# Kernel optimization log

Measured on AMD Instinct MI355X. Metric: run time of the kernel, lower is better.

## Reference

```python
import jax, jax.numpy as jnp
import numpy as np


def axisangle2mat(p):
    # p: [N, 6] = (rotation vector rx,ry,rz, translation tx,ty,tz) -> [N, 3, 4]
    v = p[:, :3]
    t = p[:, 3:]
    theta = jnp.sqrt(jnp.sum(v * v, axis=-1) + 1e-12)  # [N]
    k = v / theta[:, None]
    kx, ky, kz = k[:, 0], k[:, 1], k[:, 2]
    zero = jnp.zeros_like(kx)
    K = jnp.stack([
        jnp.stack([zero, -kz, ky], -1),
        jnp.stack([kz, zero, -kx], -1),
        jnp.stack([-ky, kx, zero], -1),
    ], -2)  # [N,3,3]
    I = jnp.eye(3, dtype=p.dtype)
    s = jnp.sin(theta)[:, None, None]
    c = (1.0 - jnp.cos(theta))[:, None, None]
    R = I + s * K + c * jnp.matmul(K, K)
    return jnp.concatenate([R, t[:, :, None]], axis=-1)  # [N,3,4]


def grid_sample_3d(vol, grid):
    # vol: [D,H,W]; grid: [...,3] with last dim (x,y,z) in [-1,1].
    # Replicates F.grid_sample(mode='bilinear', padding_mode='zeros', align_corners=False).
    D, H, W = vol.shape
    ix = ((grid[..., 0] + 1.0) * W - 1.0) * 0.5
    iy = ((grid[..., 1] + 1.0) * H - 1.0) * 0.5
    iz = ((grid[..., 2] + 1.0) * D - 1.0) * 0.5
    x0 = jnp.floor(ix); y0 = jnp.floor(iy); z0 = jnp.floor(iz)
    fx = ix - x0; fy = iy - y0; fz = iz - z0
    vol_flat = vol.reshape(-1)
    out = jnp.zeros(grid.shape[:-1], vol.dtype)
    for dz in (0, 1):
        for dy in (0, 1):
            for dx in (0, 1):
                xc = x0 + dx; yc = y0 + dy; zc = z0 + dz
                wgt = ((fx if dx else 1.0 - fx) * (fy if dy else 1.0 - fy) * (fz if dz else 1.0 - fz))
                valid = ((xc >= 0) & (xc < W) & (yc >= 0) & (yc < H) & (zc >= 0) & (zc < D))
                xi = jnp.clip(xc, 0, W - 1).astype(jnp.int32)
                yi = jnp.clip(yc, 0, H - 1).astype(jnp.int32)
                zi = jnp.clip(zc, 0, D - 1).astype(jnp.int32)
                v = vol_flat[(zi * H + yi) * W + xi]
                out = out + jnp.where(valid, v * wgt, 0.0)
    return out


def setup_inputs() -> dict:
    key = jax.random.key(0)
    ks = jax.random.split(key, 8)
    B, n, D, H, W = 4096, 2048, 256, 256, 256
    x = jax.random.normal(ks[0], (1, 1, D, H, W), dtype=jnp.float32)
    # voxel-space sample points inside the volume
    sampleGrid = jax.random.uniform(ks[1], (B, 3), dtype=jnp.float32) * jnp.array([W - 1, H - 1, D - 1], jnp.float32)
    ax = jnp.concatenate([
        jax.random.normal(ks[2], (B, 1, 3), dtype=jnp.float32) * 0.1,   # small rotations
        jax.random.normal(ks[3], (B, 1, 3), dtype=jnp.float32) * 5.0,   # translations (voxels)
    ], axis=-1)
    low = jax.random.uniform(ks[4], (B, 1, 3), dtype=jnp.float32) * 2.0
    ext = jax.random.uniform(ks[5], (B, 1, 3), dtype=jnp.float32) * 4.0 + 1.0
    bound = jnp.concatenate([low, low + ext], axis=1)  # [B,2,3], bound[:,1] > bound[:,0]
    A = jax.random.normal(ks[6], (B, 3, 3), dtype=jnp.float32) * 0.3
    InvCovScaled = jnp.einsum('bij,bkj->bik', A, A) + 0.5 * jnp.eye(3, dtype=jnp.float32)  # SPD
    xyz_psf = jax.random.normal(ks[7], (B, n, 3), dtype=jnp.float32)
    psf_sigma = jnp.ones((1,), jnp.float32)  # unused in forward (as in the original)
    return dict(x=x, sampleGrid=sampleGrid, ax=ax, bound=bound,
                InvCovScaled=InvCovScaled, psf_sigma=psf_sigma, xyz_psf=xyz_psf)


def reference(x, sampleGrid, ax, bound, InvCovScaled, psf_sigma, xyz_psf):
    # x: [1,1,D,H,W]; sampleGrid: [B,3]; ax: [B,1,6]; bound: [B,2,3];
    # InvCovScaled: [B,3,3]; xyz_psf: [B,n,3] (the torch.randn draw, made explicit)
    W = x.shape[-1]; H = x.shape[-2]; D = x.shape[-3]
    size = (W, H, D)  # matches torch: size = [x.shape[-1], x.shape[-2], x.shape[-3]]
    scaled_xyz_psf = 2.0 * jax.nn.sigmoid(xyz_psf) - 1.0                      # [B,n,3]
    half = (bound[:, 1, :] - bound[:, 0, :]) * 0.5                            # [B,3]
    bound_psf = scaled_xyz_psf * half[:, None]                                # [B,n,3]
    mat = axisangle2mat(ax.reshape(-1, 6)).reshape(ax.shape[:-1] + (3, 4))    # [B,1,3,4]
    R = mat[:, 0, :, :3]                                                      # [B,3,3]
    T = mat[:, 0, :, 3]                                                       # [B,3]
    # trans_first=True: R @ (p + T)
    mat_sampleGrid = jnp.einsum('bij,bj->bi', R, sampleGrid + T)[:, None]     # [B,1,3]
    psf_sampleGrid = mat_sampleGrid + bound_psf                               # [B,n,3]
    norm = jnp.array([size[0] - 1, size[1] - 1, size[2] - 1], psf_sampleGrid.dtype)
    grid = 2.0 * (psf_sampleGrid / norm - 0.5)
    psf_x = grid_sample_3d(x[0, 0], grid)                                     # [B,n]
    # Mahalanobis-style weights: exp(-0.5 * c^T InvCov c)
    q = jnp.einsum('bni,bij,bnj->bn', bound_psf, InvCovScaled, bound_psf)
    w = jnp.exp(-0.5 * q)                                                     # [B,n]
    y = jnp.sum(psf_x * w, axis=-1) / jnp.sum(w, axis=-1)                     # [B]
    return y
```

## Files before the change

kernel.cpp:

```cpp
#include <hip/hip_runtime.h>
#include <math.h>

constexpr int NT   = 256;
constexpr int DIMV = 256;
constexpr int RS   = 8;
constexpr int RROW = 9;
constexpr int RSLICE = RS * RROW;

__device__ __forceinline__ float rflf(float x) {
    return __uint_as_float(__builtin_amdgcn_readfirstlane(__float_as_uint(x)));
}
__device__ __forceinline__ float fexp2(float x) {
#if __has_builtin(__builtin_amdgcn_exp2f)
    return __builtin_amdgcn_exp2f(x);
#else
    return __expf(x * 0.6931471805599453f);
#endif
}

__global__ __launch_bounds__(NT, 6) void psf_sample_kernel(
    const float* __restrict__ vol,
    const float* __restrict__ sampleGrid,
    const float* __restrict__ ax,
    const float* __restrict__ bound,
    const float* __restrict__ invcov,
    const float* __restrict__ xyz,
    float* __restrict__ out,
    int n)
{
    const int b   = blockIdx.x;
    const int tid = threadIdx.x;

    __shared__ float s_vol[RS * RSLICE];
    __shared__ float s_red[2 * (NT / 64)];

    const float v0 = ax[b*6+0], v1 = ax[b*6+1], v2 = ax[b*6+2];
    const float t0 = ax[b*6+3], t1 = ax[b*6+4], t2 = ax[b*6+5];
    const float theta = sqrtf(v0*v0 + v1*v1 + v2*v2 + 1e-12f);
    const float inv = 1.0f / theta;
    const float kx = v0*inv, ky = v1*inv, kz = v2*inv;
    const float sn = sinf(theta);
    const float cn = 1.0f - cosf(theta);
    const float R00 = 1.0f - cn*(ky*ky + kz*kz);
    const float R01 = -sn*kz + cn*kx*ky;
    const float R02 =  sn*ky + cn*kx*kz;
    const float R10 =  sn*kz + cn*kx*ky;
    const float R11 = 1.0f - cn*(kx*kx + kz*kz);
    const float R12 = -sn*kx + cn*ky*kz;
    const float R20 = -sn*ky + cn*kx*kz;
    const float R21 =  sn*kx + cn*ky*kz;
    const float R22 = 1.0f - cn*(kx*kx + ky*ky);
    const float g0 = sampleGrid[b*3+0] + t0;
    const float g1 = sampleGrid[b*3+1] + t1;
    const float g2 = sampleGrid[b*3+2] + t2;
    const float ms0 = R00*g0 + R01*g1 + R02*g2;
    const float ms1 = R10*g0 + R11*g1 + R12*g2;
    const float ms2 = R20*g0 + R21*g1 + R22*g2;
    const float h0 = (bound[b*6+3] - bound[b*6+0]) * 0.5f;
    const float h1 = (bound[b*6+4] - bound[b*6+1]) * 0.5f;
    const float h2 = (bound[b*6+5] - bound[b*6+2]) * 0.5f;
    const float M00 = invcov[b*9+0], M01 = invcov[b*9+1], M02 = invcov[b*9+2];
    const float M11 = invcov[b*9+4], M12 = invcov[b*9+5], M22 = invcov[b*9+8];

    const float LOG2E = 1.4426950408889634f;
    const float Bxx = rflf(-0.5f * M00 * h0 * h0 * LOG2E);
    const float Byy = rflf(-0.5f * M11 * h1 * h1 * LOG2E);
    const float Bzz = rflf(-0.5f * M22 * h2 * h2 * LOG2E);
    const float Bxy = rflf(-M01 * h0 * h1 * LOG2E);
    const float Bxz = rflf(-M02 * h0 * h2 * LOG2E);
    const float Byz = rflf(-M12 * h1 * h2 * LOG2E);

    const float kk = 256.0f / 255.0f;
    const float cix = rflf(fmaf(ms0, kk, -0.5f));
    const float ciy = rflf(fmaf(ms1, kk, -0.5f));
    const float ciz = rflf(fmaf(ms2, kk, -0.5f));
    const float hx = rflf(h0 * kk);
    const float hy = rflf(h1 * kk);
    const float hz = rflf(h2 * kk);

    const int bx = __builtin_amdgcn_readfirstlane((int)floorf(cix - hx - 1e-3f));
    const int by = __builtin_amdgcn_readfirstlane((int)floorf(ciy - hy - 1e-3f));
    const int bz = __builtin_amdgcn_readfirstlane((int)floorf(ciz - hz - 1e-3f));
    const float addrC = rflf((float)(bz * RSLICE + by * RROW + bx));
    const bool fast = (hx <= 2.9f) && (hy <= 2.9f) && (hz <= 2.9f);

    if (fast) {
        #pragma unroll
        for (int pass = 0; pass < (RS*RS*RS)/NT; ++pass) {
            const int idx = pass * NT + tid;
            const int lx = idx & 7, ly = (idx >> 3) & 7, lz = idx >> 6;
            const int gx = bx + lx, gy = by + ly, gz = bz + lz;
            float v = 0.0f;
            if ((unsigned)gx < (unsigned)DIMV && (unsigned)gy < (unsigned)DIMV &&
                (unsigned)gz < (unsigned)DIMV)
                v = vol[((size_t)gz * DIMV + gy) * DIMV + gx];
            s_vol[(lz * RS + ly) * RROW + lx] = v;
        }
    }
    __syncthreads();

    float sum_wx = 0.0f, sum_w = 0.0f;

    auto doSample = [&](float rx, float ry, float rz) {
        const float ex = fexp2(rx * -LOG2E);
        const float ey = fexp2(ry * -LOG2E);
        const float ez = fexp2(rz * -LOG2E);
        const float sx = (1.0f - ex) * __builtin_amdgcn_rcpf(1.0f + ex);
        const float sy = (1.0f - ey) * __builtin_amdgcn_rcpf(1.0f + ey);
        const float sz = (1.0f - ez) * __builtin_amdgcn_rcpf(1.0f + ez);

        const float ixf = fmaf(sx, hx, cix);
        const float iyf = fmaf(sy, hy, ciy);
        const float izf = fmaf(sz, hz, ciz);
        const float x0f = floorf(ixf), y0f = floorf(iyf), z0f = floorf(izf);
        const float fx = ixf - x0f, fy = iyf - y0f, fz = izf - z0f;

        float val;
        if (fast) {
            const float ef = fmaf(z0f, (float)RSLICE,
                             fmaf(y0f, (float)RROW, x0f - addrC));
            const int e = (int)ef;
            const float* p = &s_vol[e];
            const float v000 = p[0],              v001 = p[1];
            const float v010 = p[RROW],           v011 = p[RROW + 1];
            const float v100 = p[RSLICE],         v101 = p[RSLICE + 1];
            const float v110 = p[RSLICE + RROW],  v111 = p[RSLICE + RROW + 1];
            const float a00 = fmaf(fx, v001 - v000, v000);
            const float a01 = fmaf(fx, v011 - v010, v010);
            const float a10 = fmaf(fx, v101 - v100, v100);
            const float a11 = fmaf(fx, v111 - v110, v110);
            const float a0  = fmaf(fy, a01 - a00, a00);
            const float a1  = fmaf(fy, a11 - a10, a10);
            val = fmaf(fz, a1 - a0, a0);
        } else {
            const int x0 = (int)x0f, y0 = (int)y0f, z0 = (int)z0f;
            const int x1 = x0 + 1, y1 = y0 + 1, z1 = z0 + 1;
            const bool vx0 = (unsigned)x0 < (unsigned)DIMV;
            const bool vx1 = (unsigned)x1 < (unsigned)DIMV;
            const bool vy0 = (unsigned)y0 < (unsigned)DIMV;
            const bool vy1 = (unsigned)y1 < (unsigned)DIMV;
            const bool vz0 = (unsigned)z0 < (unsigned)DIMV;
            const bool vz1 = (unsigned)z1 < (unsigned)DIMV;
            const int cx0 = min(max(x0,0),DIMV-1), cx1 = min(max(x1,0),DIMV-1);
            const int cy0 = min(max(y0,0),DIMV-1), cy1 = min(max(y1,0),DIMV-1);
            const int cz0 = min(max(z0,0),DIMV-1), cz1 = min(max(z1,0),DIMV-1);
            const float wx0 = 1.0f-fx, wx1 = fx, wy0 = 1.0f-fy, wy1 = fy;
            const float wz0 = 1.0f-fz, wz1 = fz;
            const int r00 = (cz0*DIMV + cy0)*DIMV, r01 = (cz0*DIMV + cy1)*DIMV;
            const int r10 = (cz1*DIMV + cy0)*DIMV, r11 = (cz1*DIMV + cy1)*DIMV;
            val  = (vz0&&vy0&&vx0) ? vol[r00+cx0]*(wz0*wy0*wx0) : 0.0f;
            val += (vz0&&vy0&&vx1) ? vol[r00+cx1]*(wz0*wy0*wx1) : 0.0f;
            val += (vz0&&vy1&&vx0) ? vol[r01+cx0]*(wz0*wy1*wx0) : 0.0f;
            val += (vz0&&vy1&&vx1) ? vol[r01+cx1]*(wz0*wy1*wx1) : 0.0f;
            val += (vz1&&vy0&&vx0) ? vol[r10+cx0]*(wz1*wy0*wx0) : 0.0f;
            val += (vz1&&vy0&&vx1) ? vol[r10+cx1]*(wz1*wy0*wx1) : 0.0f;
            val += (vz1&&vy1&&vx0) ? vol[r11+cx0]*(wz1*wy1*wx0) : 0.0f;
            val += (vz1&&vy1&&vx1) ? vol[r11+cx1]*(wz1*wy1*wx1) : 0.0f;
        }

        const float f = fmaf(Bxx, sx*sx,
                        fmaf(Byy, sy*sy,
                        fmaf(Bzz, sz*sz,
                        fmaf(Bxy, sx*sy,
                        fmaf(Bxz, sx*sz, Byz * (sy*sz))))));
        const float w = fexp2(f);
        sum_w  += w;
        sum_wx = fmaf(w, val, sum_wx);
    };

    const int ng = n >> 2;
    const float4* __restrict__ xb4 =
        reinterpret_cast<const float4*>(xyz + (size_t)b * n * 3);
    for (int g = tid; g < ng; g += 2*NT) {
        const float4 a0 = xb4[g*3 + 0];
        const float4 a1 = xb4[g*3 + 1];
        const float4 a2 = xb4[g*3 + 2];
        const int g2 = g + NT;
        const bool has2 = g2 < ng;
        float4 c0, c1, c2;
        if (has2) { c0 = xb4[g2*3 + 0]; c1 = xb4[g2*3 + 1]; c2 = xb4[g2*3 + 2]; }
        doSample(a0.x, a0.y, a0.z);
        doSample(a0.w, a1.x, a1.y);
        doSample(a1.z, a1.w, a2.x);
        doSample(a2.y, a2.z, a2.w);
        if (has2) {
            doSample(c0.x, c0.y, c0.z);
            doSample(c0.w, c1.x, c1.y);
            doSample(c1.z, c1.w, c2.x);
            doSample(c2.y, c2.z, c2.w);
        }
    }
    const float* __restrict__ xb = xyz + (size_t)b * n * 3;
    for (int i = (ng << 2) + tid; i < n; i += NT)
        doSample(xb[i*3+0], xb[i*3+1], xb[i*3+2]);

    #pragma unroll
    for (int off = 32; off > 0; off >>= 1) {
        sum_wx += __shfl_down(sum_wx, off);
        sum_w  += __shfl_down(sum_w,  off);
    }
    const int wave = tid >> 6;
    const int lane = tid & 63;
    if (lane == 0) { s_red[wave*2] = sum_wx; s_red[wave*2+1] = sum_w; }
    __syncthreads();
    if (tid == 0) {
        float twx = 0.0f, tw = 0.0f;
        #pragma unroll
        for (int wv = 0; wv < NT/64; ++wv) { twx += s_red[wv*2]; tw += s_red[wv*2+1]; }
        out[b] = twx / tw;
    }
}

extern "C" void kernel_launch(void* const* d_in, const int* in_sizes, int n_in,
                              void* d_out, int out_size, void* d_ws, size_t ws_size,
                              hipStream_t stream) {
    const float* vol        = (const float*)d_in[0];
    const float* sampleGrid = (const float*)d_in[1];
    const float* ax         = (const float*)d_in[2];
    const float* bound      = (const float*)d_in[3];
    const float* invcov     = (const float*)d_in[4];
    const float* xyz        = (const float*)d_in[6];
    float* out              = (float*)d_out;

    const int B = in_sizes[1] / 3;
    const int n = in_sizes[6] / (B * 3);

    psf_sample_kernel<<<B, NT, 0, stream>>>(vol, sampleGrid, ax, bound, invcov,
                                            xyz, out, n);
}
```

Baseline: 30.74 us.

## Assign one wavefront per batch element instead of one block per element

Each 256-thread block now handles four batch elements, one per wavefront. Each wave loads its own 8x8x8 shared-memory volume patch and reduces with shuffles only, so the cross-wave shared-memory reduction and second barrier go away. The grid shrinks by four and each wave processes all 2048 samples of its element serially across 64 lanes. Launch bounds drop the occupancy hint from 6 to 4 blocks. The gain is less per-block setup and synchronisation, at the cost of longer per-wave work and possibly different latency hiding.

```diff
diff --git a/kernel.cpp b/kernel.cpp
--- a/kernel.cpp
+++ b/kernel.cpp
@@ -2,6 +2,7 @@
 #include <math.h>
 
 constexpr int NT   = 256;
+constexpr int WPB  = 4;
 constexpr int DIMV = 256;
 constexpr int RS   = 8;
 constexpr int RROW = 9;
@@ -18,7 +19,7 @@
 #endif
 }
 
-__global__ __launch_bounds__(NT, 6) void psf_sample_kernel(
+__global__ __launch_bounds__(NT, 4) void psf_sample_kernel(
     const float* __restrict__ vol,
     const float* __restrict__ sampleGrid,
     const float* __restrict__ ax,
@@ -26,188 +27,182 @@
     const float* __restrict__ invcov,
     const float* __restrict__ xyz,
     float* __restrict__ out,
-    int n)
+    int n, int B)
 {
-    const int b   = blockIdx.x;
-    const int tid = threadIdx.x;
-
-    __shared__ float s_vol[RS * RSLICE];
-    __shared__ float s_red[2 * (NT / 64)];
-
-    const float v0 = ax[b*6+0], v1 = ax[b*6+1], v2 = ax[b*6+2];
-    const float t0 = ax[b*6+3], t1 = ax[b*6+4], t2 = ax[b*6+5];
-    const float theta = sqrtf(v0*v0 + v1*v1 + v2*v2 + 1e-12f);
-    const float inv = 1.0f / theta;
-    const float kx = v0*inv, ky = v1*inv, kz = v2*inv;
-    const float sn = sinf(theta);
-    const float cn = 1.0f - cosf(theta);
-    const float R00 = 1.0f - cn*(ky*ky + kz*kz);
-    const float R01 = -sn*kz + cn*kx*ky;
-    const float R02 =  sn*ky + cn*kx*kz;
-    const float R10 =  sn*kz + cn*kx*ky;
-    const float R11 = 1.0f - cn*(kx*kx + kz*kz);
-    const float R12 = -sn*kx + cn*ky*kz;
-    const float R20 = -sn*ky + cn*kx*kz;
-    const float R21 =  sn*kx + cn*ky*kz;
-    const float R22 = 1.0f - cn*(kx*kx + ky*ky);
-    const float g0 = sampleGrid[b*3+0] + t0;
-    const float g1 = sampleGrid[b*3+1] + t1;
-    const float g2 = sampleGrid[b*3+2] + t2;
-    const float ms0 = R00*g0 + R01*g1 + R02*g2;
-    const float ms1 = R10*g0 + R11*g1 + R12*g2;
-    const float ms2 = R20*g0 + R21*g1 + R22*g2;
-    const float h0 = (bound[b*6+3] - bound[b*6+0]) * 0.5f;
-    const float h1 = (bound[b*6+4] - bound[b*6+1]) * 0.5f;
-    const float h2 = (bound[b*6+5] - bound[b*6+2]) * 0.5f;
-    const float M00 = invcov[b*9+0], M01 = invcov[b*9+1], M02 = invcov[b*9+2];
-    const float M11 = invcov[b*9+4], M12 = invcov[b*9+5], M22 = invcov[b*9+8];
+    const int tid  = threadIdx.x;
+    const int wid  = tid >> 6;
+    const int lane = tid & 63;
+    const int b    = blockIdx.x * WPB + wid;
+    const bool valid = b < B;
+
+    __shared__ float s_vol[WPB][RS * RSLICE];
 
     const float LOG2E = 1.4426950408889634f;
-    const float Bxx = rflf(-0.5f * M00 * h0 * h0 * LOG2E);
-    const float Byy = rflf(-0.5f * M11 * h1 * h1 * LOG2E);
-    const float Bzz = rflf(-0.5f * M22 * h2 * h2 * LOG2E);
-    const float Bxy = rflf(-M01 * h0 * h1 * LOG2E);
-    const float Bxz = rflf(-M02 * h0 * h2 * LOG2E);
-    const float Byz = rflf(-M12 * h1 * h2 * LOG2E);
-
-    const float kk = 256.0f / 255.0f;
-    const float cix = rflf(fmaf(ms0, kk, -0.5f));
-    const float ciy = rflf(fmaf(ms1, kk, -0.5f));
-    const float ciz = rflf(fmaf(ms2, kk, -0.5f));
-    const float hx = rflf(h0 * kk);
-    const float hy = rflf(h1 * kk);
-    const float hz = rflf(h2 * kk);
-
-    const int bx = __builtin_amdgcn_readfirstlane((int)floorf(cix - hx - 1e-3f));
-    const int by = __builtin_amdgcn_readfirstlane((int)floorf(ciy - hy - 1e-3f));
-    const int bz = __builtin_amdgcn_readfirstlane((int)floorf(ciz - hz - 1e-3f));
-    const float addrC = rflf((float)(bz * RSLICE + by * RROW + bx));
-    const bool fast = (hx <= 2.9f) && (hy <= 2.9f) && (hz <= 2.9f);
-
-    if (fast) {
-        #pragma unroll
-        for (int pass = 0; pass < (RS*RS*RS)/NT; ++pass) {
-            const int idx = pass * NT + tid;
-            const int lx = idx & 7, ly = (idx >> 3) & 7, lz = idx >> 6;
-            const int gx = bx + lx, gy = by + ly, gz = bz + lz;
-            float v = 0.0f;
-            if ((unsigned)gx < (unsigned)DIMV && (unsigned)gy < (unsigned)DIMV &&
-                (unsigned)gz < (unsigned)DIMV)
-                v = vol[((size_t)gz * DIMV + gy) * DIMV + gx];
-            s_vol[(lz * RS + ly) * RROW + lx] = v;
+    float cix, ciy, ciz, hx, hy, hz, addrC;
+    float Bxx, Byy, Bzz, Bxy, Bxz, Byz;
+    int bx = 0, by = 0, bz = 0;
+    bool fast = false;
+    float h0 = 0, h1 = 0, h2 = 0;
+
+    if (valid) {
+        const float v0 = ax[b*6+0], v1 = ax[b*6+1], v2 = ax[b*6+2];
+        const float t0 = ax[b*6+3], t1 = ax[b*6+4], t2 = ax[b*6+5];
+        const float theta = sqrtf(v0*v0 + v1*v1 + v2*v2 + 1e-12f);
+        const float inv = 1.0f / theta;
+        const float kx = v0*inv, ky = v1*inv, kz = v2*inv;
+        const float sn = sinf(theta);
+        const float cn = 1.0f - cosf(theta);
+        const float R00 = 1.0f - cn*(ky*ky + kz*kz);
+        const float R01 = -sn*kz + cn*kx*ky;
+        const float R02 =  sn*ky + cn*kx*kz;
+        const float R10 =  sn*kz + cn*kx*ky;
+        const float R11 = 1.0f - cn*(kx*kx + kz*kz);
+        const float R12 = -sn*kx + cn*ky*kz;
+        const float R20 = -sn*ky + cn*kx*kz;
+        const float R21 =  sn*kx + cn*ky*kz;
+        const float R22 = 1.0f - cn*(kx*kx + ky*ky);
+        const float g0 = sampleGrid[b*3+0] + t0;
+        const float g1 = sampleGrid[b*3+1] + t1;
+        const float g2 = sampleGrid[b*3+2] + t2;
+        const float ms0 = R00*g0 + R01*g1 + R02*g2;
+        const float ms1 = R10*g0 + R11*g1 + R12*g2;
+        const float ms2 = R20*g0 + R21*g1 + R22*g2;
+        h0 = (bound[b*6+3] - bound[b*6+0]) * 0.5f;
+        h1 = (bound[b*6+4] - bound[b*6+1]) * 0.5f;
+        h2 = (bound[b*6+5] - bound[b*6+2]) * 0.5f;
+        const float M00 = invcov[b*9+0], M01 = invcov[b*9+1], M02 = invcov[b*9+2];
+        const float M11 = invcov[b*9+4], M12 = invcov[b*9+5], M22 = invcov[b*9+8];
+
+        Bxx = rflf(-0.5f * M00 * h0 * h0 * LOG2E);
+        Byy = rflf(-0.5f * M11 * h1 * h1 * LOG2E);
+        Bzz = rflf(-0.5f * M22 * h2 * h2 * LOG2E);
+        Bxy = rflf(-M01 * h0 * h1 * LOG2E);
+        Bxz = rflf(-M02 * h0 * h2 * LOG2E);
+        Byz = rflf(-M12 * h1 * h2 * LOG2E);
+
+        const float kk = 256.0f / 255.0f;
+        cix = rflf(fmaf(ms0, kk, -0.5f));
+        ciy = rflf(fmaf(ms1, kk, -0.5f));
+        ciz = rflf(fmaf(ms2, kk, -0.5f));
+        hx  = rflf(h0 * kk);
+        hy  = rflf(h1 * kk);
+        hz  = rflf(h2 * kk);
+
+        bx = __builtin_amdgcn_readfirstlane((int)floorf(cix - hx - 1e-3f));
+        by = __builtin_amdgcn_readfirstlane((int)floorf(ciy - hy - 1e-3f));
+        bz = __builtin_amdgcn_readfirstlane((int)floorf(ciz - hz - 1e-3f));
+        addrC = rflf((float)(bz * RSLICE + by * RROW + bx));
+        fast = (hx <= 2.9f) && (hy <= 2.9f) && (hz <= 2.9f);
+
+        if (fast) {
+            #pragma unroll
+            for (int pass = 0; pass < (RS*RS*RS)/64; ++pass) {
+                const int idx = pass * 64 + lane;
+                const int lx = idx & 7, ly = (idx >> 3) & 7, lz = idx >> 6;
+                const int gx = bx + lx, gy = by + ly, gz = bz + lz;
+                float v = 0.0f;
+                if ((unsigned)gx < (unsigned)DIMV && (unsigned)gy < (unsigned)DIMV &&
+                    (unsigned)gz < (unsigned)DIMV)
+                    v = vol[((size_t)gz * DIMV + gy) * DIMV + gx];
+                s_vol[wid][(lz * RS + ly) * RROW + lx] = v;
+            }
         }
     }
     __syncthreads();
 
-    float sum_wx = 0.0f, sum_w = 0.0f;
-
-    auto doSample = [&](float rx, float ry, float rz) {
-        const float ex = fexp2(rx * -LOG2E);
-        const float ey = fexp2(ry * -LOG2E);
-        const float ez = fexp2(rz * -LOG2E);
-        const float sx = (1.0f - ex) * __builtin_amdgcn_rcpf(1.0f + ex);
-        const float sy = (1.0f - ey) * __builtin_amdgcn_rcpf(1.0f + ey);
-        const float sz = (1.0f - ez) * __builtin_amdgcn_rcpf(1.0f + ez);
-
-        const float ixf = fmaf(sx, hx, cix);
-        const float iyf = fmaf(sy, hy, ciy);
-        const float izf = fmaf(sz, hz, ciz);
-        const float x0f = floorf(ixf), y0f = floorf(iyf), z0f = floorf(izf);
-        const float fx = ixf - x0f, fy = iyf - y0f, fz = izf - z0f;
-
-        float val;
-        if (fast) {
-            const float ef = fmaf(z0f, (float)RSLICE,
-                             fmaf(y0f, (float)RROW, x0f - addrC));
-            const int e = (int)ef;
-            const float* p = &s_vol[e];
-            const float v000 = p[0],              v001 = p[1];
-            const float v010 = p[RROW],           v011 = p[RROW + 1];
-            const float v100 = p[RSLICE],         v101 = p[RSLICE + 1];
-            const float v110 = p[RSLICE + RROW],  v111 = p[RSLICE + RROW + 1];
-            const float a00 = fmaf(fx, v001 - v000, v000);
-            const float a01 = fmaf(fx, v011 - v010, v010);
-            const float a10 = fmaf(fx, v101 - v100, v100);
-            const float a11 = fmaf(fx, v111 - v110, v110);
-            const float a0  = fmaf(fy, a01 - a00, a00);
-            const float a1  = fmaf(fy, a11 - a10, a10);
-            val = fmaf(fz, a1 - a0, a0);
-        } else {
-            const int x0 = (int)x0f, y0 = (int)y0f, z0 = (int)z0f;
-            const int x1 = x0 + 1, y1 = y0 + 1, z1 = z0 + 1;
-            const bool vx0 = (unsigned)x0 < (unsigned)DIMV;
-            const bool vx1 = (unsigned)x1 < (unsigned)DIMV;
-            const bool vy0 = (unsigned)y0 < (unsigned)DIMV;
-            const bool vy1 = (unsigned)y1 < (unsigned)DIMV;
-            const bool vz0 = (unsigned)z0 < (unsigned)DIMV;
-            const bool vz1 = (unsigned)z1 < (unsigned)DIMV;
-            const int cx0 = min(max(x0,0),DIMV-1), cx1 = min(max(x1,0),DIMV-1);
-            const int cy0 = min(max(y0,0),DIMV-1), cy1 = min(max(y1,0),DIMV-1);
-            const int cz0 = min(max(z0,0),DIMV-1), cz1 = min(max(z1,0),DIMV-1);
-            const float wx0 = 1.0f-fx, wx1 = fx, wy0 = 1.0f-fy, wy1 = fy;
-            const float wz0 = 1.0f-fz, wz1 = fz;
-            const int r00 = (cz0*DIMV + cy0)*DIMV, r01 = (cz0*DIMV + cy1)*DIMV;
-            const int r10 = (cz1*DIMV + cy0)*DIMV, r11 = (cz1*DIMV + cy1)*DIMV;
-            val  = (vz0&&vy0&&vx0) ? vol[r00+cx0]*(wz0*wy0*wx0) : 0.0f;
-            val += (vz0&&vy0&&vx1) ? vol[r00+cx1]*(wz0*wy0*wx1) : 0.0f;
-            val += (vz0&&vy1&&vx0) ? vol[r01+cx0]*(wz0*wy1*wx0) : 0.0f;
-            val += (vz0&&vy1&&vx1) ? vol[r01+cx1]*(wz0*wy1*wx1) : 0.0f;
-            val += (vz1&&vy0&&vx0) ? vol[r10+cx0]*(wz1*wy0*wx0) : 0.0f;
-            val += (vz1&&vy0&&vx1) ? vol[r10+cx1]*(wz1*wy0*wx1) : 0.0f;
-            val += (vz1&&vy1&&vx0) ? vol[r11+cx0]*(wz1*wy1*wx0) : 0.0f;
-            val += (vz1&&vy1&&vx1) ? vol[r11+cx1]*(wz1*wy1*wx1) : 0.0f;
+    if (valid) {
+        float sum_wx = 0.0f, sum_w = 0.0f;
+        const float* __restrict__ sreg = s_vol[wid];
+
+        auto doSample = [&](float rx, float ry, float rz) {
+            const float ex = fexp2(rx * -LOG2E);
+            const float ey = fexp2(ry * -LOG2E);
+            const float ez = fexp2(rz * -LOG2E);
+            const float sx = (1.0f - ex) * __builtin_amdgcn_rcpf(1.0f + ex);
+            const float sy = (1.0f - ey) * __builtin_amdgcn_rcpf(1.0f + ey);
+            const float sz = (1.0f - ez) * __builtin_amdgcn_rcpf(1.0f + ez);
+
+            const float ixf = fmaf(sx, hx, cix);
+            const float iyf = fmaf(sy, hy, ciy);
+            const float izf = fmaf(sz, hz, ciz);
+            const float x0f = floorf(ixf), y0f = floorf(iyf), z0f = floorf(izf);
+            const float fx = ixf - x0f, fy = iyf - y0f, fz = izf - z0f;
+
+            float val;
+            if (fast) {
+                const float ef = fmaf(z0f, (float)RSLICE,
+                                 fmaf(y0f, (float)RROW, x0f - addrC));
+                const int e = (int)ef;
+                const float* p = &sreg[e];
+                const float v000 = p[0],              v001 = p[1];
+                const float v010 = p[RROW],           v011 = p[RROW + 1];
+                const float v100 = p[RSLICE],         v101 = p[RSLICE + 1];
+                const float v110 = p[RSLICE + RROW],  v111 = p[RSLICE + RROW + 1];
+                const float a00 = fmaf(fx, v001 - v000, v000);
+                const float a01 = fmaf(fx, v011 - v010, v010);
+                const float a10 = fmaf(fx, v101 - v100, v100);
+                const float a11 = fmaf(fx, v111 - v110, v110);
+                const float a0  = fmaf(fy, a01 - a00, a00);
+                const float a1  = fmaf(fy, a11 - a10, a10);
+                val = fmaf(fz, a1 - a0, a0);
+            } else {
+                const int x0 = (int)x0f, y0 = (int)y0f, z0 = (int)z0f;
+                const int x1 = x0 + 1, y1 = y0 + 1, z1 = z0 + 1;
+                const bool vx0 = (unsigned)x0 < (unsigned)DIMV;
+                const bool vx1 = (unsigned)x1 < (unsigned)DIMV;
+                const bool vy0 = (unsigned)y0 < (unsigned)DIMV;
+                const bool vy1 = (unsigned)y1 < (unsigned)DIMV;
+                const bool vz0 = (unsigned)z0 < (unsigned)DIMV;
+                const bool vz1 = (unsigned)z1 < (unsigned)DIMV;
+                const int cx0 = min(max(x0,0),DIMV-1), cx1 = min(max(x1,0),DIMV-1);
+                const int cy0 = min(max(y0,0),DIMV-1), cy1 = min(max(y1,0),DIMV-1);
+                const int cz0 = min(max(z0,0),DIMV-1), cz1 = min(max(z1,0),DIMV-1);
+                const float wx0 = 1.0f-fx, wx1 = fx, wy0 = 1.0f-fy, wy1 = fy;
+                const float wz0 = 1.0f-fz, wz1 = fz;
+                const int r00 = (cz0*DIMV + cy0)*DIMV, r01 = (cz0*DIMV + cy1)*DIMV;
+                const int r10 = (cz1*DIMV + cy0)*DIMV, r11 = (cz1*DIMV + cy1)*DIMV;
+                val  = (vz0&&vy0&&vx0) ? vol[r00+cx0]*(wz0*wy0*wx0) : 0.0f;
+                val += (vz0&&vy0&&vx1) ? vol[r00+cx1]*(wz0*wy0*wx1) : 0.0f;
+                val += (vz0&&vy1&&vx0) ? vol[r01+cx0]*(wz0*wy1*wx0) : 0.0f;
+                val += (vz0&&vy1&&vx1) ? vol[r01+cx1]*(wz0*wy1*wx1) : 0.0f;
+                val += (vz1&&vy0&&vx0) ? vol[r10+cx0]*(wz1*wy0*wx0) : 0.0f;
+                val += (vz1&&vy0&&vx1) ? vol[r10+cx1]*(wz1*wy0*wx1) : 0.0f;
+                val += (vz1&&vy1&&vx0) ? vol[r11+cx0]*(wz1*wy1*wx0) : 0.0f;
+                val += (vz1&&vy1&&vx1) ? vol[r11+cx1]*(wz1*wy1*wx1) : 0.0f;
+            }
+
+            const float f = fmaf(Bxx, sx*sx,
+                            fmaf(Byy, sy*sy,
+                            fmaf(Bzz, sz*sz,
+                            fmaf(Bxy, sx*sy,
+                            fmaf(Bxz, sx*sz, Byz * (sy*sz))))));
+            const float w = fexp2(f);
+            sum_w  += w;
+            sum_wx = fmaf(w, val, sum_wx);
+        };
+
+        const int ng = n >> 2;
+        const float4* __restrict__ xb4 =
+            reinterpret_cast<const float4*>(xyz + (size_t)b * n * 3);
+        for (int g = lane; g < ng; g += 64) {
+            const float4 q0 = xb4[g*3 + 0];
+            const float4 q1 = xb4[g*3 + 1];
+            const float4 q2 = xb4[g*3 + 2];
+            doSample(q0.x, q0.y, q0.z);
+            doSample(q0.w, q1.x, q1.y);
+            doSample(q1.z, q1.w, q2.x);
+            doSample(q2.y, q2.z, q2.w);
         }
-
-        const float f = fmaf(Bxx, sx*sx,
-                        fmaf(Byy, sy*sy,
-                        fmaf(Bzz, sz*sz,
-                        fmaf(Bxy, sx*sy,
-                        fmaf(Bxz, sx*sz, Byz * (sy*sz))))));
-        const float w = fexp2(f);
-        sum_w  += w;
-        sum_wx = fmaf(w, val, sum_wx);
-    };
-
-    const int ng = n >> 2;
-    const float4* __restrict__ xb4 =
-        reinterpret_cast<const float4*>(xyz + (size_t)b * n * 3);
-    for (int g = tid; g < ng; g += 2*NT) {
-        const float4 a0 = xb4[g*3 + 0];
-        const float4 a1 = xb4[g*3 + 1];
-        const float4 a2 = xb4[g*3 + 2];
-        const int g2 = g + NT;
-        const bool has2 = g2 < ng;
-        float4 c0, c1, c2;
-        if (has2) { c0 = xb4[g2*3 + 0]; c1 = xb4[g2*3 + 1]; c2 = xb4[g2*3 + 2]; }
-        doSample(a0.x, a0.y, a0.z);
-        doSample(a0.w, a1.x, a1.y);
-        doSample(a1.z, a1.w, a2.x);
-        doSample(a2.y, a2.z, a2.w);
-        if (has2) {
-            doSample(c0.x, c0.y, c0.z);
-            doSample(c0.w, c1.x, c1.y);
-            doSample(c1.z, c1.w, c2.x);
-            doSample(c2.y, c2.z, c2.w);
+        const float* __restrict__ xb = xyz + (size_t)b * n * 3;
+        for (int i = (ng << 2) + lane; i < n; i += 64)
+            doSample(xb[i*3+0], xb[i*3+1], xb[i*3+2]);
+
+        #pragma unroll
+        for (int off = 32; off > 0; off >>= 1) {
+            sum_wx += __shfl_down(sum_wx, off);
+            sum_w  += __shfl_down(sum_w,  off);
         }
-    }
-    const float* __restrict__ xb = xyz + (size_t)b * n * 3;
-    for (int i = (ng << 2) + tid; i < n; i += NT)
-        doSample(xb[i*3+0], xb[i*3+1], xb[i*3+2]);
-
-    #pragma unroll
-    for (int off = 32; off > 0; off >>= 1) {
-        sum_wx += __shfl_down(sum_wx, off);
-        sum_w  += __shfl_down(sum_w,  off);
-    }
-    const int wave = tid >> 6;
-    const int lane = tid & 63;
-    if (lane == 0) { s_red[wave*2] = sum_wx; s_red[wave*2+1] = sum_w; }
-    __syncthreads();
-    if (tid == 0) {
-        float twx = 0.0f, tw = 0.0f;
-        #pragma unroll
-        for (int wv = 0; wv < NT/64; ++wv) { twx += s_red[wv*2]; tw += s_red[wv*2+1]; }
-        out[b] = twx / tw;
+        if (lane == 0) out[b] = sum_wx / sum_w;
     }
 }
 
@@ -225,6 +220,7 @@
     const int B = in_sizes[1] / 3;
     const int n = in_sizes[6] / (B * 3);
 
-    psf_sample_kernel<<<B, NT, 0, stream>>>(vol, sampleGrid, ax, bound, invcov,
-                                            xyz, out, n);
-}
+    const int grid = (B + WPB - 1) / WPB;
+    psf_sample_kernel<<<grid, NT, 0, stream>>>(vol, sampleGrid, ax, bound,
+                                               invcov, xyz, out, n, B);
+}
```

Measured after the change: 29.15 us. 5.2% less time.
